# Kernel tuning notes

Hardware: AMD Instinct MI355X
Metric: run time of the kernel (lower is better)

Reference implementation:

```python
import jax, jax.numpy as jnp
import numpy as np
import math

B, T, D, H = 2, 4096, 1024, 16
DH = D // H
LOCAL = 3
MAX_GATE = 0.6


def dilated_positions(seq_len, local=LOCAL):
    A = local + int(math.ceil(math.log2(max(seq_len, 2)))) + 1
    pos = np.zeros((seq_len, A), np.int32)
    msk = np.zeros((seq_len, A), bool)
    for i in range(seq_len):
        ap = [i] + [i - j for j in range(1, local + 1) if i - j >= 0]
        k = 2
        while 2 ** k <= i:
            ap.append(i - 2 ** k)
            k += 1
        pos[i, :len(ap)] = ap
        msk[i, :len(ap)] = True
    return pos, msk


def pid_proj(x, Wp, Wi, Wd, Wg, bg):
    # x: (B,T,D); W*: (D,D); Wg: (D,3); bg: (3,)
    t = x.shape[1]
    denom = jnp.arange(1, t + 1, dtype=x.dtype)[None, :, None]
    integral = jnp.cumsum(x, axis=1) / denom
    derivative = jnp.concatenate([jnp.zeros_like(x[:, :1]), x[:, 1:] - x[:, :-1]], axis=1)
    g = jax.nn.softmax(x @ Wg + bg, axis=-1)
    g = jnp.minimum(g, MAX_GATE)
    g = g / g.sum(axis=-1, keepdims=True)
    return g[..., 0:1] * (x @ Wp) + g[..., 1:2] * (integral @ Wi) + g[..., 2:3] * (derivative @ Wd)


def setup_inputs() -> dict:
    key = jax.random.key(0)
    ks = jax.random.split(key, 16)
    s = 1.0 / math.sqrt(D)
    inp = {"x": jax.random.normal(ks[0], (B, T, D), jnp.float32)}
    i = 1
    for name in ("q", "k", "v"):
        inp[f"Wp_{name}"] = jax.random.normal(ks[i], (D, D), jnp.float32) * s; i += 1
        inp[f"Wi_{name}"] = jax.random.normal(ks[i], (D, D), jnp.float32) * s * 0.3; i += 1
        inp[f"Wd_{name}"] = jax.random.normal(ks[i], (D, D), jnp.float32) * s * 0.3; i += 1
        inp[f"Wg_{name}"] = jax.random.normal(ks[i], (D, 3), jnp.float32) * s; i += 1
        inp[f"bg_{name}"] = jnp.array([0.5, 0.0, 0.0], jnp.float32)
    inp["Wo"] = jax.random.normal(ks[13], (D, D), jnp.float32) * s
    pos, msk = dilated_positions(T)
    inp["positions"] = jnp.asarray(pos)
    inp["mask"] = jnp.asarray(msk)
    return inp


def reference(x, Wp_q, Wi_q, Wd_q, Wg_q, bg_q,
              Wp_k, Wi_k, Wd_k, Wg_k, bg_k,
              Wp_v, Wi_v, Wd_v, Wg_v, bg_v,
              Wo, positions, mask):
    b, t, d = x.shape
    scale = DH ** -0.5
    def heads(y):  # (B,T,D) -> (B,H,T,DH)
        return y.reshape(b, t, H, DH).transpose(0, 2, 1, 3)
    q = heads(pid_proj(x, Wp_q, Wi_q, Wd_q, Wg_q, bg_q))
    k = heads(pid_proj(x, Wp_k, Wi_k, Wd_k, Wg_k, bg_k))
    v = heads(pid_proj(x, Wp_v, Wi_v, Wd_v, Wg_v, bg_v))
    # gather per-query sparse K/V: (B,H,T,A,DH)
    k_sparse = k[:, :, positions]
    v_sparse = v[:, :, positions]
    scores = jnp.einsum('bhsd,bhsad->bhsa', q, k_sparse) * scale
    scores = jnp.where(mask[None, None], scores, -jnp.inf)
    attn = jax.nn.softmax(scores, axis=-1)
    out = jnp.einsum('bhsa,bhsad->bhsd', attn, v_sparse)
    out = out.transpose(0, 2, 1, 3).reshape(b, t, d)
    return out @ Wo
```

## Files before the change

kernel.cpp:

```cpp
#include <hip/hip_runtime.h>
#include <hip/hip_bf16.h>
#include <cstdint>

#define B_   2
#define T_   4096
#define D_   1024
#define H_   16
#define DH_  64
#define M_   (B_*T_)
#define K3_  (3*D_)
#define TC_  128
#define NCH_ (T_/TC_)

typedef __attribute__((ext_vector_type(4))) float  f32x4;
typedef __attribute__((ext_vector_type(8))) short  short8;

__device__ __forceinline__ float bf2f(ushort u) {
    union { uint32_t i; float f; } v; v.i = ((uint32_t)u) << 16; return v.f;
}
__device__ __forceinline__ ushort f2bf(float f) {
    union { float f; uint32_t i; } v; v.f = f;
    uint32_t r = v.i + 0x7FFF + ((v.i >> 16) & 1);
    return (ushort)(r >> 16);
}

template<bool F32>
__device__ __forceinline__ float ld_in(const void* p, size_t i) {
    if (F32) return ((const float*)p)[i];
    return bf2f(((const ushort*)p)[i]);
}

__device__ __forceinline__ void st_c(ushort* p, float v) { *p = f2bf(v); }
__device__ __forceinline__ void st_c(float*  p, float v) { *p = v; }

#define GLOAD_LDS16(g, l) \
    __builtin_amdgcn_global_load_lds((const __attribute__((address_space(1))) void*)(g), \
                                     (__attribute__((address_space(3))) void*)(l), 16, 0, 0)

__global__ void detect_kernel(const ushort* __restrict__ xu, int* __restrict__ flag) {
    __shared__ int cnt;
    if (threadIdx.x == 0) cnt = 0;
    __syncthreads();
    int c = 0;
    for (int i = threadIdx.x; i < 16384; i += 256) {
        ushort u = xu[i];
        if ((u & 0x7F80) == 0x7F80) c++;
    }
    if (c) atomicAdd(&cnt, c);
    __syncthreads();
    if (threadIdx.x == 0) flag[0] = (cnt > 0) ? 1 : 0;
}

template<bool F32>
__device__ __forceinline__ void gates_body(const void* x,
                                           const void* Wg_q, const void* bg_q,
                                           const void* Wg_k, const void* bg_k,
                                           const void* Wg_v, const void* bg_v,
                                           float* __restrict__ g9) {
    const int wave = threadIdx.x >> 6, lane = threadIdx.x & 63;
    const int row  = blockIdx.x * 4 + wave;
    const size_t xoff = (size_t)row * D_;
    float acc[9] = {0,0,0,0,0,0,0,0,0};
    for (int d = lane; d < D_; d += 64) {
        float xv = ld_in<F32>(x, xoff + d);
        #pragma unroll
        for (int c = 0; c < 3; c++) {
            acc[0+c] += xv * ld_in<F32>(Wg_q, d*3+c);
            acc[3+c] += xv * ld_in<F32>(Wg_k, d*3+c);
            acc[6+c] += xv * ld_in<F32>(Wg_v, d*3+c);
        }
    }
    #pragma unroll
    for (int i = 0; i < 9; i++) {
        #pragma unroll
        for (int o = 32; o >= 1; o >>= 1) acc[i] += __shfl_xor(acc[i], o, 64);
    }
    const void* bgs[3] = {bg_q, bg_k, bg_v};
    float g[9];
    #pragma unroll
    for (int p = 0; p < 3; p++) {
        float l0 = acc[p*3+0] + ld_in<F32>(bgs[p], 0);
        float l1 = acc[p*3+1] + ld_in<F32>(bgs[p], 1);
        float l2 = acc[p*3+2] + ld_in<F32>(bgs[p], 2);
        float mx = fmaxf(l0, fmaxf(l1, l2));
        float e0 = expf(l0-mx), e1 = expf(l1-mx), e2 = expf(l2-mx);
        float s  = e0+e1+e2;
        float g0 = fminf(e0/s, 0.6f), g1 = fminf(e1/s, 0.6f), g2 = fminf(e2/s, 0.6f);
        float s2 = g0+g1+g2;
        g0 /= s2; g1 /= s2; g2 /= s2;
        float g1c = fmaxf(g1, 1e-30f), g2c = fmaxf(g2, 1e-30f);
        g[p*3+0] = g0 / g1c;
        g[p*3+1] = g1c / g2c;
        g[p*3+2] = g2c;
    }
    if (lane == 0) {
        #pragma unroll
        for (int i = 0; i < 9; i++) g9[(size_t)row*9 + i] = g[i];
    }
}
__global__ void gates_kernel(const void* x,
                             const void* Wg_q, const void* bg_q,
                             const void* Wg_k, const void* bg_k,
                             const void* Wg_v, const void* bg_v,
                             const int* __restrict__ flag, float* __restrict__ g9) {
    if (flag[0]) gates_body<true >(x, Wg_q, bg_q, Wg_k, bg_k, Wg_v, bg_v, g9);
    else         gates_body<false>(x, Wg_q, bg_q, Wg_k, bg_k, Wg_v, bg_v, g9);
}

template<bool F32>
__device__ __forceinline__ void chunk_sum_body(const void* x, float* __restrict__ part) {
    const int d = blockIdx.x * 256 + threadIdx.x;
    const int tc = blockIdx.y, b = blockIdx.z;
    const size_t base = ((size_t)b*T_ + (size_t)tc*TC_) * D_ + d;
    float s = 0.f;
    for (int i = 0; i < TC_; i++) s += ld_in<F32>(x, base + (size_t)i * D_);
    part[((size_t)b*NCH_ + tc) * D_ + d] = s;
}
__global__ void chunk_sum_kernel(const void* x, const int* __restrict__ flag,
                                 float* __restrict__ part) {
    if (flag[0]) chunk_sum_body<true >(x, part);
    else         chunk_sum_body<false>(x, part);
}

__global__ void scan_part_kernel(float* __restrict__ part) {
    const int idx = blockIdx.x * 256 + threadIdx.x;
    const int b = idx >> 10, d = idx & (D_-1);
    float run = 0.f;
    for (int tc = 0; tc < NCH_; tc++) {
        size_t o = ((size_t)b*NCH_ + tc) * D_ + d;
        float v = part[o]; part[o] = run; run += v;
    }
}

template<bool F32>
__device__ __forceinline__ void build_xs_body(const void* x, const float* __restrict__ part,
                                              ushort* __restrict__ Xc) {
    const int d0 = (blockIdx.x * 256 + threadIdx.x) * 2;
    const int tc = blockIdx.y, b = blockIdx.z;
    const int t0 = tc * TC_;
    float carry0 = part[((size_t)b*NCH_ + tc) * D_ + d0];
    float carry1 = part[((size_t)b*NCH_ + tc) * D_ + d0 + 1];
    const size_t xbase = ((size_t)b*T_ + t0) * D_ + d0;
    float prev0 = (t0 > 0) ? ld_in<F32>(x, xbase - D_)     : 0.0f;
    float prev1 = (t0 > 0) ? ld_in<F32>(x, xbase - D_ + 1) : 0.0f;
    for (int i = 0; i < TC_; i++) {
        const int t = t0 + i;
        float xv0 = ld_in<F32>(x, xbase + (size_t)i * D_);
        float xv1 = ld_in<F32>(x, xbase + (size_t)i * D_ + 1);
        carry0 += xv0; carry1 += xv1;
        const float rinv = 1.0f / (float)(t + 1);
        float in0 = carry0 * rinv, in1 = carry1 * rinv;
        float de0 = (t == 0) ? 0.0f : (xv0 - prev0);
        float de1 = (t == 0) ? 0.0f : (xv1 - prev1);
        prev0 = xv0; prev1 = xv1;
        const size_t base = ((size_t)b*T_ + t) * K3_ + d0;
        *(ushort2*)(Xc + base       ) = make_ushort2(f2bf(xv0), f2bf(xv1));
        *(ushort2*)(Xc + base +   D_) = make_ushort2(f2bf(in0), f2bf(in1));
        *(ushort2*)(Xc + base + 2*D_) = make_ushort2(f2bf(de0), f2bf(de1));
    }
}
__global__ void build_xs_kernel(const void* x, const float* __restrict__ part,
                                const int* __restrict__ flag, ushort* __restrict__ Xc) {
    if (flag[0]) build_xs_body<true >(x, part, Xc);
    else         build_xs_body<false>(x, part, Xc);
}

struct WPtrs { const void* w[10]; };
template<bool F32>
__device__ __forceinline__ void transpose_w_body(WPtrs ptrs, ushort* __restrict__ Wt,
                                                 ushort* __restrict__ WoT) {
    const int z = blockIdx.z;
    const void* src = ptrs.w[z];
    __shared__ float tile[32][33];
    const int tx = threadIdx.x & 31, ty = threadIdx.x >> 5;
    const int d0 = blockIdx.x * 32, c0 = blockIdx.y * 32;
    #pragma unroll
    for (int i = 0; i < 4; i++) {
        int r = ty + i*8;
        tile[r][tx] = ld_in<F32>(src, (size_t)(d0 + r) * D_ + c0 + tx);
    }
    __syncthreads();
    if (z < 9) {
        const int p = z / 3, j = z % 3;
        #pragma unroll
        for (int i = 0; i < 4; i++) {
            int r = ty + i*8;
            Wt[(size_t)(p*D_ + c0 + r) * K3_ + j*D_ + d0 + tx] = f2bf(tile[tx][r]);
        }
    } else {
        #pragma unroll
        for (int i = 0; i < 4; i++) {
            int r = ty + i*8;
            WoT[(size_t)(c0 + r) * D_ + d0 + tx] = f2bf(tile[tx][r]);
        }
    }
}
__global__ void transpose_w_kernel(WPtrs ptrs, const int* __restrict__ flag,
                                   ushort* __restrict__ Wt, ushort* __restrict__ WoT) {
    if (flag[0]) transpose_w_body<true >(ptrs, Wt, WoT);
    else         transpose_w_body<false>(ptrs, Wt, WoT);
}

template<typename CT, int NT, bool GATED>
__global__ __launch_bounds__(256) void gemm_bt_kernel(
        const ushort* __restrict__ Abase,
        const ushort* __restrict__ Bt,
        CT* __restrict__ C,
        const float* __restrict__ g9,
        int K, int lda, int ldc) {
    __shared__ __align__(16) ushort As[128*64];
    __shared__ __align__(16) ushort Bs[128*64];
    const int tid  = threadIdx.x;
    const int lane = tid & 63;
    const int wave = tid >> 6;

    const int gid = blockIdx.x;
    const int grp = gid / (16*NT);
    const int rem = gid % (16*NT);
    const int mt  = grp*16 + (rem & 15);
    const int nt  = rem >> 4;
    const int m0 = mt * 128;
    const int n0 = nt * 128;
    const int p  = nt >> 3;

    const ushort* agp[4]; const ushort* bgp[4];
    ushort* alp[4]; ushort* blp[4];
    #pragma unroll
    for (int g = 0; g < 4; g++) {
        const int I   = g*256 + tid;
        const int row = I >> 3;
        const int c8  = (I & 7) ^ (row & 7);
        agp[g] = Abase + (size_t)(m0 + row) * lda + c8*8;
        bgp[g] = Bt    + (size_t)(n0 + row) * K   + c8*8;
        alp[g] = As + (size_t)I * 8;
        blp[g] = Bs + (size_t)I * 8;
    }

    const int wm = wave & 1, wn = wave >> 1;
    const int quad = lane >> 4, l16 = lane & 15;
    const int sw = l16 & 7;

    f32x4 acc[4][4] = {};

    const int NSEG = GATED ? 3 : 1;
    const int SEG  = K / NSEG;
    for (int seg = 0; seg < NSEG; seg++) {
        for (int kt = seg*SEG; kt < (seg+1)*SEG; kt += 64) {
            #pragma unroll
            for (int g = 0; g < 4; g++) GLOAD_LDS16(agp[g] + kt, alp[g]);
            #pragma unroll
            for (int g = 0; g < 4; g++) GLOAD_LDS16(bgp[g] + kt, blp[g]);
            __syncthreads();
            #pragma unroll
            for (int kk = 0; kk < 2; kk++) {
                short8 af[4], bfr[4];
                #pragma unroll
                for (int i = 0; i < 4; i++) {
                    const int r = wm*64 + i*16 + l16;
                    af[i]  = *(const short8*)(As + (size_t)(r*8 + ((quad + kk*4) ^ sw)) * 8);
                }
                #pragma unroll
                for (int j = 0; j < 4; j++) {
                    const int r = wn*64 + j*16 + l16;
                    bfr[j] = *(const short8*)(Bs + (size_t)(r*8 + ((quad + kk*4) ^ sw)) * 8);
                }
                #pragma unroll
                for (int i = 0; i < 4; i++)
                    #pragma unroll
                    for (int j = 0; j < 4; j++)
                        acc[i][j] = __builtin_amdgcn_mfma_f32_16x16x32_bf16(af[i], bfr[j], acc[i][j], 0, 0, 0);
            }
            __syncthreads();
        }
        if (GATED) {
            #pragma unroll
            for (int i = 0; i < 4; i++) {
                float gv[4];
                #pragma unroll
                for (int rg = 0; rg < 4; rg++) {
                    const int rrow = m0 + wm*64 + i*16 + quad*4 + rg;
                    gv[rg] = g9[(size_t)rrow * 9 + p*3 + seg];
                }
                #pragma unroll
                for (int j = 0; j < 4; j++)
                    #pragma unroll
                    for (int rg = 0; rg < 4; rg++)
                        acc[i][j][rg] *= gv[rg];
            }
        }
    }
    #pragma unroll
    for (int i = 0; i < 4; i++) {
        #pragma unroll
        for (int j = 0; j < 4; j++) {
            const int rrow = m0 + wm*64 + i*16 + quad*4;
            const int col  = n0 + wn*64 + j*16 + l16;
            #pragma unroll
            for (int rg = 0; rg < 4; rg++)
                st_c(&C[(size_t)(rrow + rg) * ldc + col], acc[i][j][rg]);
        }
    }
}

__global__ __launch_bounds__(256) void attn_kernel(const ushort* __restrict__ QKV,
                                                   ushort* __restrict__ AO) {
    const int tid = threadIdx.x;
    const int bt  = blockIdx.x;
    const int t   = bt & (T_-1);
    const size_t qrow = (size_t)bt * K3_;
    const int e0 = tid * 4;

    const ushort4 q4 = *(const ushort4*)(QKV + qrow + e0);
    const float qf0 = bf2f(q4.x), qf1 = bf2f(q4.y), qf2 = bf2f(q4.z), qf3 = bf2f(q4.w);

    float sc[14];
    #pragma unroll
    for (int a = 0; a < 14; a++) {
        const int off = (a <= 3) ? a : (1 << (a - 2));
        float p = -1e30f;
        if (off <= t) {
            const ushort4 k4 = *(const ushort4*)(QKV + qrow - (size_t)off*K3_ + D_ + e0);
            float pp = qf0*bf2f(k4.x) + qf1*bf2f(k4.y) + qf2*bf2f(k4.z) + qf3*bf2f(k4.w);
            pp += __shfl_xor(pp, 1, 64);
            pp += __shfl_xor(pp, 2, 64);
            pp += __shfl_xor(pp, 4, 64);
            pp += __shfl_xor(pp, 8, 64);
            p = pp * 0.125f;
        }
        sc[a] = p;
    }
    float mx = -1e30f;
    #pragma unroll
    for (int a = 0; a < 14; a++) mx = fmaxf(mx, sc[a]);
    float ev[14], s = 0.0f;
    #pragma unroll
    for (int a = 0; a < 14; a++) { ev[a] = (sc[a] > -1e29f) ? expf(sc[a] - mx) : 0.0f; s += ev[a]; }
    const float rs = 1.0f / s;

    float a0 = 0.f, a1 = 0.f, a2 = 0.f, a3 = 0.f;
    #pragma unroll
    for (int a = 0; a < 14; a++) {
        const int off = (a <= 3) ? a : (1 << (a - 2));
        if (off <= t) {
            const ushort4 v4 = *(const ushort4*)(QKV + qrow - (size_t)off*K3_ + 2*D_ + e0);
            const float w = ev[a] * rs;
            a0 += w * bf2f(v4.x); a1 += w * bf2f(v4.y);
            a2 += w * bf2f(v4.z); a3 += w * bf2f(v4.w);
        }
    }
    ushort* dst = AO + (size_t)bt * D_ + e0;
    dst[0] = f2bf(a0); dst[1] = f2bf(a1); dst[2] = f2bf(a2); dst[3] = f2bf(a3);
}

extern "C" void kernel_launch(void* const* d_in, const int* in_sizes, int n_in,
                              void* d_out, int out_size, void* d_ws, size_t ws_size,
                              hipStream_t stream) {
    (void)in_sizes; (void)n_in; (void)out_size; (void)ws_size;
    const void* x    = d_in[0];
    const void* Wg_q = d_in[4];  const void* bg_q = d_in[5];
    const void* Wg_k = d_in[9];  const void* bg_k = d_in[10];
    const void* Wg_v = d_in[14]; const void* bg_v = d_in[15];

    char* ws = (char*)d_ws;
    int*    flag = (int*)ws;    ws += 16;
    float*  g9   = (float*)ws;  ws += (size_t)M_*9*4;
    float*  part = (float*)ws;  ws += (size_t)B_*NCH_*D_*4;
    ushort* Wt   = (ushort*)ws; ws += (size_t)K3_*K3_*2;
    ushort* WoT  = (ushort*)ws; ws += (size_t)D_*D_*2;
    ushort* Xc   = (ushort*)ws; ws += (size_t)M_*K3_*2;
    ushort* QKV  = (ushort*)ws; ws += (size_t)M_*K3_*2;
    ushort* AO   = (ushort*)ws; ws += (size_t)M_*D_*2;

    detect_kernel<<<1, 256, 0, stream>>>((const ushort*)x, flag);
    gates_kernel<<<M_/4, 256, 0, stream>>>(x, Wg_q, bg_q, Wg_k, bg_k, Wg_v, bg_v, flag, g9);
    chunk_sum_kernel<<<dim3(D_/256, NCH_, B_), 256, 0, stream>>>(x, flag, part);
    scan_part_kernel<<<(B_*D_)/256, 256, 0, stream>>>(part);
    WPtrs wp;
    wp.w[0] = d_in[1];  wp.w[1] = d_in[2];  wp.w[2] = d_in[3];
    wp.w[3] = d_in[6];  wp.w[4] = d_in[7];  wp.w[5] = d_in[8];
    wp.w[6] = d_in[11]; wp.w[7] = d_in[12]; wp.w[8] = d_in[13];
    wp.w[9] = d_in[16];
    transpose_w_kernel<<<dim3(32, 32, 10), 256, 0, stream>>>(wp, flag, Wt, WoT);
    build_xs_kernel<<<dim3(D_/512, NCH_, B_), 256, 0, stream>>>(x, part, flag, Xc);
    gemm_bt_kernel<ushort, 24, true><<<24*64, 256, 0, stream>>>(Xc, Wt, QKV, g9, K3_, K3_, K3_);
    attn_kernel<<<B_*T_, 256, 0, stream>>>(QKV, AO);
    gemm_bt_kernel<float, 8, false><<<8*64, 256, 0, stream>>>(AO, WoT, (float*)d_out, nullptr, D_, D_, D_);
}
```

Before: 547.8 us.

## Rewrite GEMM as 8-wave 128x256 tile with triple-buffered LDS pipeline

```diff
diff --git a/kernel.cpp b/kernel.cpp
--- a/kernel.cpp
+++ b/kernel.cpp
@@ -201,78 +201,129 @@
     else         transpose_w_body<false>(ptrs, Wt, WoT);
 }
 
-template<typename CT, int NT, bool GATED>
-__global__ __launch_bounds__(256) void gemm_bt_kernel(
+template<typename CT, int NTILES, bool GATED>
+__global__ __launch_bounds__(512, 2) void gemm_bt8_kernel(
         const ushort* __restrict__ Abase,
         const ushort* __restrict__ Bt,
         CT* __restrict__ C,
         const float* __restrict__ g9,
         int K, int lda, int ldc) {
-    __shared__ __align__(16) ushort As[128*64];
-    __shared__ __align__(16) ushort Bs[128*64];
+    __shared__ __align__(16) ushort LDS[3 * 24576];
     const int tid  = threadIdx.x;
     const int lane = tid & 63;
     const int wave = tid >> 6;
-
-    const int gid = blockIdx.x;
-    const int grp = gid / (16*NT);
-    const int rem = gid % (16*NT);
-    const int mt  = grp*16 + (rem & 15);
-    const int nt  = rem >> 4;
+    const int wm   = wave >> 2;
+    const int wn   = wave & 3;
+    const int quad = lane >> 4, l16 = lane & 15, sw = l16 & 7;
+
+    const int MT     = M_ / 128;
+    const int cpx    = (MT * NTILES) / 8;
+    const int wg     = (blockIdx.x % 8) * cpx + blockIdx.x / 8;
+    const int mchunk = MT / 8;
+    const int rem    = wg % (mchunk * NTILES);
+    const int mt     = (wg / (mchunk * NTILES)) * mchunk + (rem % mchunk);
+    const int nt     = rem / mchunk;
     const int m0 = mt * 128;
-    const int n0 = nt * 128;
-    const int p  = nt >> 3;
-
-    const ushort* agp[4]; const ushort* bgp[4];
-    ushort* alp[4]; ushort* blp[4];
+    const int n0 = nt * 256;
+    const int p  = n0 >> 10;
+
+    const ushort* asrc[2]; int aoff[2];
+    #pragma unroll
+    for (int g = 0; g < 2; g++) {
+        const int I = g*512 + tid;
+        const int row = I >> 3, c8 = (I & 7) ^ (row & 7);
+        asrc[g] = Abase + (size_t)(m0 + row) * lda + c8*8;
+        aoff[g] = I * 8;
+    }
+    const ushort* bsrc[4]; int boff[4];
     #pragma unroll
     for (int g = 0; g < 4; g++) {
-        const int I   = g*256 + tid;
-        const int row = I >> 3;
-        const int c8  = (I & 7) ^ (row & 7);
-        agp[g] = Abase + (size_t)(m0 + row) * lda + c8*8;
-        bgp[g] = Bt    + (size_t)(n0 + row) * K   + c8*8;
-        alp[g] = As + (size_t)I * 8;
-        blp[g] = Bs + (size_t)I * 8;
-    }
-
-    const int wm = wave & 1, wn = wave >> 1;
-    const int quad = lane >> 4, l16 = lane & 15;
-    const int sw = l16 & 7;
-
+        const int I = g*512 + tid;
+        const int row = I >> 3, c8 = (I & 7) ^ (row & 7);
+        bsrc[g] = Bt + (size_t)(n0 + row) * K + c8*8;
+        boff[g] = I * 8;
+    }
+    int ard[4], brd[4];
+    #pragma unroll
+    for (int i = 0; i < 4; i++) {
+        ard[i] = (wm*64 + i*16 + l16) * 64;
+        brd[i] = (wn*64 + i*16 + l16) * 64;
+    }
+
+    const int NKT = K >> 6;
     f32x4 acc[4][4] = {};
 
-    const int NSEG = GATED ? 3 : 1;
-    const int SEG  = K / NSEG;
-    for (int seg = 0; seg < NSEG; seg++) {
-        for (int kt = seg*SEG; kt < (seg+1)*SEG; kt += 64) {
+    #pragma unroll
+    for (int g = 0; g < 2; g++) GLOAD_LDS16(asrc[g], &LDS[aoff[g]]);
+    #pragma unroll
+    for (int g = 0; g < 4; g++) GLOAD_LDS16(bsrc[g], &LDS[8192 + boff[g]]);
+    #pragma unroll
+    for (int g = 0; g < 2; g++) GLOAD_LDS16(asrc[g] + 64, &LDS[24576 + aoff[g]]);
+    #pragma unroll
+    for (int g = 0; g < 4; g++) GLOAD_LDS16(bsrc[g] + 64, &LDS[24576 + 8192 + boff[g]]);
+    asm volatile("s_waitcnt vmcnt(6)" ::: "memory");
+    __builtin_amdgcn_s_barrier();
+
+    for (int t = 0; t < NKT; ++t) {
+        const int cur = t % 3;
+        const int ab  = cur * 24576;
+        const int bb  = ab + 8192;
+        const bool do_stage = (t + 2 < NKT);
+        const int sb  = ((t + 2) % 3) * 24576;
+        const int skt = (t + 2) << 6;
+
+        short8 af[4], bfr[4];
+
+        #pragma unroll
+        for (int i = 0; i < 4; i++)
+            af[i]  = *(const short8*)&LDS[ab + ard[i] + (quad ^ sw) * 8];
+        #pragma unroll
+        for (int j = 0; j < 4; j++)
+            bfr[j] = *(const short8*)&LDS[bb + brd[j] + (quad ^ sw) * 8];
+        if (do_stage) {
+            GLOAD_LDS16(asrc[0] + skt, &LDS[sb + aoff[0]]);
+            GLOAD_LDS16(asrc[1] + skt, &LDS[sb + aoff[1]]);
+            GLOAD_LDS16(bsrc[0] + skt, &LDS[sb + 8192 + boff[0]]);
+        }
+        __builtin_amdgcn_s_barrier();
+        asm volatile("s_waitcnt lgkmcnt(0)" ::: "memory");
+        __builtin_amdgcn_sched_barrier(0);
+        __builtin_amdgcn_s_setprio(1);
+        #pragma unroll
+        for (int i = 0; i < 4; i++)
             #pragma unroll
-            for (int g = 0; g < 4; g++) GLOAD_LDS16(agp[g] + kt, alp[g]);
+            for (int j = 0; j < 4; j++)
+                acc[i][j] = __builtin_amdgcn_mfma_f32_16x16x32_bf16(af[i], bfr[j], acc[i][j], 0, 0, 0);
+        __builtin_amdgcn_s_setprio(0);
+        __builtin_amdgcn_s_barrier();
+
+        #pragma unroll
+        for (int i = 0; i < 4; i++)
+            af[i]  = *(const short8*)&LDS[ab + ard[i] + ((quad + 4) ^ sw) * 8];
+        #pragma unroll
+        for (int j = 0; j < 4; j++)
+            bfr[j] = *(const short8*)&LDS[bb + brd[j] + ((quad + 4) ^ sw) * 8];
+        if (do_stage) {
+            GLOAD_LDS16(bsrc[1] + skt, &LDS[sb + 8192 + boff[1]]);
+            GLOAD_LDS16(bsrc[2] + skt, &LDS[sb + 8192 + boff[2]]);
+            GLOAD_LDS16(bsrc[3] + skt, &LDS[sb + 8192 + boff[3]]);
+        }
+        __builtin_amdgcn_s_barrier();
+        asm volatile("s_waitcnt lgkmcnt(0)" ::: "memory");
+        __builtin_amdgcn_sched_barrier(0);
+        __builtin_amdgcn_s_setprio(1);
+        #pragma unroll
+        for (int i = 0; i < 4; i++)
             #pragma unroll
-            for (int g = 0; g < 4; g++) GLOAD_LDS16(bgp[g] + kt, blp[g]);
-            __syncthreads();
-            #pragma unroll
-            for (int kk = 0; kk < 2; kk++) {
-                short8 af[4], bfr[4];
-                #pragma unroll
-                for (int i = 0; i < 4; i++) {
-                    const int r = wm*64 + i*16 + l16;
-                    af[i]  = *(const short8*)(As + (size_t)(r*8 + ((quad + kk*4) ^ sw)) * 8);
-                }
-                #pragma unroll
-                for (int j = 0; j < 4; j++) {
-                    const int r = wn*64 + j*16 + l16;
-                    bfr[j] = *(const short8*)(Bs + (size_t)(r*8 + ((quad + kk*4) ^ sw)) * 8);
-                }
-                #pragma unroll
-                for (int i = 0; i < 4; i++)
-                    #pragma unroll
-                    for (int j = 0; j < 4; j++)
-                        acc[i][j] = __builtin_amdgcn_mfma_f32_16x16x32_bf16(af[i], bfr[j], acc[i][j], 0, 0, 0);
-            }
-            __syncthreads();
-        }
-        if (GATED) {
+            for (int j = 0; j < 4; j++)
+                acc[i][j] = __builtin_amdgcn_mfma_f32_16x16x32_bf16(af[i], bfr[j], acc[i][j], 0, 0, 0);
+        __builtin_amdgcn_s_setprio(0);
+        if (do_stage)          asm volatile("s_waitcnt vmcnt(6)" ::: "memory");
+        else if (t + 1 < NKT)  asm volatile("s_waitcnt vmcnt(0)" ::: "memory");
+        __builtin_amdgcn_s_barrier();
+
+        if (GATED && ((t & 15) == 15)) {
+            const int seg = t >> 4;
             #pragma unroll
             for (int i = 0; i < 4; i++) {
                 float gv[4];
@@ -289,6 +340,7 @@
             }
         }
     }
+
     #pragma unroll
     for (int i = 0; i < 4; i++) {
         #pragma unroll
@@ -382,7 +434,7 @@
     wp.w[9] = d_in[16];
     transpose_w_kernel<<<dim3(32, 32, 10), 256, 0, stream>>>(wp, flag, Wt, WoT);
     build_xs_kernel<<<dim3(D_/512, NCH_, B_), 256, 0, stream>>>(x, part, flag, Xc);
-    gemm_bt_kernel<ushort, 24, true><<<24*64, 256, 0, stream>>>(Xc, Wt, QKV, g9, K3_, K3_, K3_);
+    gemm_bt8_kernel<ushort, 12, true><<<768, 512, 0, stream>>>(Xc, Wt, QKV, g9, K3_, K3_, K3_);
     attn_kernel<<<B_*T_, 256, 0, stream>>>(QKV, AO);
-    gemm_bt_kernel<float, 8, false><<<8*64, 256, 0, stream>>>(AO, WoT, (float*)d_out, nullptr, D_, D_, D_);
-}
+    gemm_bt8_kernel<float, 4, false><<<256, 512, 0, stream>>>(AO, WoT, (float*)d_out, nullptr, D_, D_, D_);
+}
```

Result: faster. 481.3 us (-12.1%).
